# Performance work log

Measured on AMD Instinct MI355X. Metric: run time of the kernel, lower is better.

## Reference

```python
import jax, jax.numpy as jnp
import numpy as np

TEMPERATURE = 0.07
EPS = 1e-12  # matches torch F.normalize eps
B, D = 16384, 128


def setup_inputs() -> dict:
    key = jax.random.key(0)
    k1, k2 = jax.random.split(key)
    anchor = jax.random.normal(k1, (B, D), dtype=jnp.float32)
    positive = jax.random.normal(k2, (B, D), dtype=jnp.float32)
    return {"anchor": anchor, "positive": positive}


def _l2_normalize(x):
    # torch F.normalize: x / max(||x||, eps)
    n = jnp.sqrt(jnp.sum(x * x, axis=-1, keepdims=True))
    return x / jnp.maximum(n, EPS)


def reference(anchor, positive):
    a = _l2_normalize(anchor)          # [B, D]
    p = _l2_normalize(positive)        # [B, D]
    pos_sim = jnp.sum(a * p, axis=-1) / TEMPERATURE            # [B]
    sim = jnp.matmul(a, p.T) / TEMPERATURE                     # [B, B]
    neg_inf = jnp.finfo(sim.dtype).min
    bsz = sim.shape[0]
    eye = jnp.eye(bsz, dtype=bool)
    neg_sim = jnp.where(eye, neg_inf, sim)                     # diag masked
    logits = jnp.concatenate([pos_sim[:, None], neg_sim], axis=1)  # [B, B+1]
    # cross-entropy with label 0: -log_softmax(logits)[:, 0]
    lse = jax.nn.logsumexp(logits, axis=1)
    loss = lse - logits[:, 0]
    return jnp.mean(loss)
```

## Files before the change

### kernel.cpp

```cpp
#include <hip/hip_runtime.h>
#include <stdint.h>

#define NROWS 16384
#define DIM 128

typedef __attribute__((ext_vector_type(8))) __bf16 bf16x8;
typedef __attribute__((ext_vector_type(4))) float f32x4;
typedef __attribute__((ext_vector_type(4))) unsigned int u32x4;

constexpr float TEMP_INV = 1.0f / 0.07f;
constexpr float LOG2E = 1.4426950408889634f;
constexpr float LN2 = 0.69314718055994531f;
constexpr float KAPPA = LOG2E * TEMP_INV;
constexpr float SQRT_KAPPA = 4.53981600f;

__device__ __forceinline__ ushort f2bf(float x) {
  uint32_t u = __builtin_bit_cast(uint32_t, x);
  uint32_t r = (u + 0x7fffu + ((u >> 16) & 1u)) >> 16;
  return (ushort)r;
}

__device__ __forceinline__ void gload_lds16(const void* g, void* l) {
  __builtin_amdgcn_global_load_lds(
      (const __attribute__((address_space(1))) unsigned int*)g,
      (__attribute__((address_space(3))) unsigned int*)l, 16, 0, 0);
}

__global__ __launch_bounds__(256) void prep_kernel(
    const float* __restrict__ anchor, const float* __restrict__ positive,
    ushort* __restrict__ abar, ushort* __restrict__ pbar,
    float* __restrict__ pos_u)
{
  const int tid = threadIdx.x;
  const int row = blockIdx.x * 16 + (tid >> 4);
  const int c0 = (tid & 15) * 8;

  const float4* a4 = reinterpret_cast<const float4*>(anchor + (size_t)row * DIM + c0);
  const float4* p4 = reinterpret_cast<const float4*>(positive + (size_t)row * DIM + c0);
  float4 a0 = a4[0], a1 = a4[1];
  float4 p0 = p4[0], p1 = p4[1];

  float af[8] = {a0.x, a0.y, a0.z, a0.w, a1.x, a1.y, a1.z, a1.w};
  float pf[8] = {p0.x, p0.y, p0.z, p0.w, p1.x, p1.y, p1.z, p1.w};

  float sa = 0.f, sp = 0.f, dp = 0.f;
#pragma unroll
  for (int j = 0; j < 8; ++j) {
    sa += af[j] * af[j];
    sp += pf[j] * pf[j];
    dp += af[j] * pf[j];
  }
#pragma unroll
  for (int m = 1; m <= 8; m <<= 1) {
    sa += __shfl_xor(sa, m, 64);
    sp += __shfl_xor(sp, m, 64);
    dp += __shfl_xor(dp, m, 64);
  }
  float inva = 1.0f / fmaxf(sqrtf(sa), 1e-12f);
  float invp = 1.0f / fmaxf(sqrtf(sp), 1e-12f);
  float ca = inva * SQRT_KAPPA;
  float cp = invp * SQRT_KAPPA;

  ushort ua[8], up[8];
#pragma unroll
  for (int j = 0; j < 8; ++j) {
    ua[j] = f2bf(af[j] * ca);
    up[j] = f2bf(pf[j] * cp);
  }
  *reinterpret_cast<uint4*>(abar + (size_t)row * DIM + c0) = *reinterpret_cast<uint4*>(ua);
  *reinterpret_cast<uint4*>(pbar + (size_t)row * DIM + c0) = *reinterpret_cast<uint4*>(up);

  if ((tid & 15) == 0)
    pos_u[row] = dp * inva * invp * KAPPA;
}

#define NSPLIT 16
#define BM 256
#define CPB (NROWS / NSPLIT)
#define BN 32
#define NIT (CPB / BN)
#define NBUF 4
#define TILE_B (BN * 256)

__global__ __launch_bounds__(256, 3) void lse_kernel(
    const ushort* __restrict__ abar,
    const ushort* __restrict__ pbar,
    float* __restrict__ sbuf )
{
  __shared__ alignas(16) char lds[NBUF][TILE_B];

  const int tid = threadIdx.x;
  const int l = tid & 63;
  const int w = tid >> 6;
  const int r15 = l & 15;
  const int hi = l >> 4;

  const int bid = blockIdx.x;
  const int csplit = bid & 15;
  const int rowblk = bid >> 4;
  const int row0 = rowblk * BM + w * 64;
  const int col0 = csplit * CPB;

  const char* abase = (const char*)abar;
  const char* pbase = (const char*)pbar;

  bf16x8 afrag[4][4];
#pragma unroll
  for (int rg = 0; rg < 4; ++rg)
#pragma unroll
    for (int kk = 0; kk < 4; ++kk) {
      size_t off = (size_t)(row0 + rg * 16 + r15) * 256 + (size_t)(kk * 32 + hi * 8) * 2;
      u32x4 v = *reinterpret_cast<const u32x4*>(abase + off);
      afrag[rg][kk] = __builtin_bit_cast(bf16x8, v);
    }

  float s[4][4];
#pragma unroll
  for (int rg = 0; rg < 4; ++rg)
#pragma unroll
    for (int rr = 0; rr < 4; ++rr) s[rg][rr] = 0.f;

  const int trow = tid >> 4;
  const size_t src0 = (size_t)(col0 + trow) * 256 + (size_t)(((tid & 15) ^ (trow & 7)) * 16);
  char* const lds0 = &lds[0][0] + w * 1024;

#define STAGE(t)                                                              \
  do {                                                                        \
    const char* gsrc = pbase + src0 + (size_t)(t) * TILE_B;                   \
    char* ld = lds0 + (size_t)((t) & 3) * TILE_B;                             \
    gload_lds16(gsrc, ld);                                                    \
    gload_lds16(gsrc + 4096, ld + 4096);                                      \
  } while (0)

  STAGE(0);
  __builtin_amdgcn_sched_barrier(0);
  STAGE(1);
  __builtin_amdgcn_sched_barrier(0);

  for (int it = 0; it < NIT; ++it) {
    if (it < NIT - 1) {
      asm volatile("s_waitcnt vmcnt(2)" ::: "memory");
    } else {
      asm volatile("s_waitcnt vmcnt(0)" ::: "memory");
    }
    __builtin_amdgcn_s_barrier();
    asm volatile("" ::: "memory");
    __builtin_amdgcn_sched_barrier(0);

    if (it + 2 < NIT) STAGE(it + 2);

    const char* bufp = &lds[0][0] + (size_t)(it & 3) * TILE_B;
#pragma unroll
    for (int ctg = 0; ctg < 2; ++ctg) {
      const int tr = ctg * 16 + r15;
      const int sw = (tr & 7) << 4;
      const char* base = bufp + tr * 256;
      bf16x8 bfrag[4];
#pragma unroll
      for (int kk = 0; kk < 4; ++kk) {
        const int cb = kk * 64 + hi * 16;
        u32x4 v = *reinterpret_cast<const u32x4*>(base + (cb ^ sw));
        bfrag[kk] = __builtin_bit_cast(bf16x8, v);
      }
      __builtin_amdgcn_s_setprio(1);
#pragma unroll
      for (int rg = 0; rg < 4; ++rg) {
        f32x4 acc = {0.f, 0.f, 0.f, 0.f};
#pragma unroll
        for (int kk = 0; kk < 4; ++kk)
          acc = __builtin_amdgcn_mfma_f32_16x16x32_bf16(afrag[rg][kk], bfrag[kk], acc, 0, 0, 0);
        s[rg][0] += __builtin_amdgcn_exp2f(acc[0]);
        s[rg][1] += __builtin_amdgcn_exp2f(acc[1]);
        s[rg][2] += __builtin_amdgcn_exp2f(acc[2]);
        s[rg][3] += __builtin_amdgcn_exp2f(acc[3]);
      }
      __builtin_amdgcn_s_setprio(0);
    }
  }
#undef STAGE

#pragma unroll
  for (int rg = 0; rg < 4; ++rg)
#pragma unroll
    for (int rr = 0; rr < 4; ++rr) {
      float v = s[rg][rr];
      v += __shfl_xor(v, 1, 64);
      v += __shfl_xor(v, 2, 64);
      v += __shfl_xor(v, 4, 64);
      v += __shfl_xor(v, 8, 64);
      if (r15 == 0) {
        int grow = row0 + rg * 16 + hi * 4 + rr;
        sbuf[(size_t)csplit * NROWS + grow] = v;
      }
    }
}

__global__ __launch_bounds__(256) void finalize1(
    const float* __restrict__ sbuf, const float* __restrict__ pos_u,
    float* __restrict__ partial)
{
  const int tid = threadIdx.x;
  const int r = blockIdx.x * 256 + tid;
  float ssum = 0.f;
#pragma unroll
  for (int c = 0; c < NSPLIT; ++c) ssum += sbuf[(size_t)c * NROWS + r];
  float acc = LN2 * (__builtin_amdgcn_logf(ssum) - pos_u[r]);
#pragma unroll
  for (int m = 1; m <= 32; m <<= 1) acc += __shfl_xor(acc, m, 64);
  __shared__ float red[4];
  if ((tid & 63) == 0) red[tid >> 6] = acc;
  __syncthreads();
  if (tid == 0) partial[blockIdx.x] = red[0] + red[1] + red[2] + red[3];
}

__global__ __launch_bounds__(64) void finalize2(
    const float* __restrict__ partial, float* __restrict__ out)
{
  float v = partial[threadIdx.x];
#pragma unroll
  for (int m = 1; m <= 32; m <<= 1) v += __shfl_xor(v, m, 64);
  if (threadIdx.x == 0) out[0] = v * (1.0f / (float)NROWS);
}

extern "C" void kernel_launch(void* const* d_in, const int* in_sizes, int n_in,
                              void* d_out, int out_size, void* d_ws, size_t ws_size,
                              hipStream_t stream) {
  const float* anchor = (const float*)d_in[0];
  const float* positive = (const float*)d_in[1];
  char* ws = (char*)d_ws;

  ushort* abar = (ushort*)ws;
  ushort* pbar = (ushort*)(ws + (size_t)NROWS * DIM * 2);
  float* pos_u = (float*)(ws + (size_t)NROWS * DIM * 4);
  float* sbuf = (float*)(ws + (size_t)NROWS * DIM * 4 + (size_t)NROWS * 4);
  float* partial = (float*)(ws + (size_t)NROWS * DIM * 4 + (size_t)NROWS * 4
                            + (size_t)NSPLIT * NROWS * 4);
  float* out = (float*)d_out;

  prep_kernel<<<NROWS / 16, 256, 0, stream>>>(anchor, positive, abar, pbar, pos_u);
  lse_kernel<<<NSPLIT * (NROWS / BM), 256, 0, stream>>>(abar, pbar, sbuf);
  finalize1<<<NROWS / 256, 256, 0, stream>>>(sbuf, pos_u, partial);
  finalize2<<<1, 64, 0, stream>>>(partial, out);
}
```

Measured before the change: 80.73 us.

## Stage P tiles in double-buffered four-tile super-iterations with fewer barriers

The LSE kernel's pipeline changes from a ring of four 8 KB tiles, with one barrier per 32-column tile, to two 32 KB halves. Each half holds four tiles and is loaded in one burst, and the kernel synchronises twice per super-iteration, so there are fewer barriers and larger asynchronous load batches. The cost is that LDS per block grows from 32 KB to 64 KB. That likely cuts the number of resident blocks per CU below the requested three, reducing latency hiding. The loads into a half are also issued only after it has been fully consumed, behind an extra barrier.

```diff
diff --git a/kernel.cpp b/kernel.cpp
--- a/kernel.cpp
+++ b/kernel.cpp
@@ -79,15 +79,17 @@
 #define CPB (NROWS / NSPLIT)
 #define BN 32
 #define NIT (CPB / BN)
-#define NBUF 4
 #define TILE_B (BN * 256)
+#define SITILES 4
+#define NSI (NIT / SITILES)
+#define HALF_B (SITILES * TILE_B)
 
 __global__ __launch_bounds__(256, 3) void lse_kernel(
     const ushort* __restrict__ abar,
     const ushort* __restrict__ pbar,
     float* __restrict__ sbuf )
 {
-  __shared__ alignas(16) char lds[NBUF][TILE_B];
+  __shared__ alignas(16) char lds[2][HALF_B];
 
   const int tid = threadIdx.x;
   const int l = tid & 63;
@@ -122,24 +124,28 @@
 
   const int trow = tid >> 4;
   const size_t src0 = (size_t)(col0 + trow) * 256 + (size_t)(((tid & 15) ^ (trow & 7)) * 16);
-  char* const lds0 = &lds[0][0] + w * 1024;
-
-#define STAGE(t)                                                              \
+  char* const ldsbase = &lds[0][0];
+  const int w1024 = w * 1024;
+
+#define STAGE_SI(si, h)                                                       \
   do {                                                                        \
-    const char* gsrc = pbase + src0 + (size_t)(t) * TILE_B;                   \
-    char* ld = lds0 + (size_t)((t) & 3) * TILE_B;                             \
-    gload_lds16(gsrc, ld);                                                    \
-    gload_lds16(gsrc + 4096, ld + 4096);                                      \
+    const char* gs = pbase + src0 + (size_t)(si) * HALF_B;                    \
+    char* ld = ldsbase + (size_t)(h) * HALF_B + w1024;                        \
+    _Pragma("unroll")                                                         \
+    for (int t = 0; t < SITILES; ++t) {                                       \
+      gload_lds16(gs + t * TILE_B, ld + t * TILE_B);                          \
+      gload_lds16(gs + t * TILE_B + 4096, ld + t * TILE_B + 4096);            \
+    }                                                                         \
   } while (0)
 
-  STAGE(0);
+  STAGE_SI(0, 0);
   __builtin_amdgcn_sched_barrier(0);
-  STAGE(1);
+  STAGE_SI(1, 1);
   __builtin_amdgcn_sched_barrier(0);
 
-  for (int it = 0; it < NIT; ++it) {
-    if (it < NIT - 1) {
-      asm volatile("s_waitcnt vmcnt(2)" ::: "memory");
+  for (int si = 0; si < NSI; ++si) {
+    if (si < NSI - 1) {
+      asm volatile("s_waitcnt vmcnt(8)" ::: "memory");
     } else {
       asm volatile("s_waitcnt vmcnt(0)" ::: "memory");
     }
@@ -147,37 +153,45 @@
     asm volatile("" ::: "memory");
     __builtin_amdgcn_sched_barrier(0);
 
-    if (it + 2 < NIT) STAGE(it + 2);
-
-    const char* bufp = &lds[0][0] + (size_t)(it & 3) * TILE_B;
-#pragma unroll
-    for (int ctg = 0; ctg < 2; ++ctg) {
-      const int tr = ctg * 16 + r15;
-      const int sw = (tr & 7) << 4;
-      const char* base = bufp + tr * 256;
-      bf16x8 bfrag[4];
-#pragma unroll
-      for (int kk = 0; kk < 4; ++kk) {
-        const int cb = kk * 64 + hi * 16;
-        u32x4 v = *reinterpret_cast<const u32x4*>(base + (cb ^ sw));
-        bfrag[kk] = __builtin_bit_cast(bf16x8, v);
+    const char* hbase = ldsbase + (size_t)(si & 1) * HALF_B;
+#pragma unroll
+    for (int tt = 0; tt < SITILES; ++tt) {
+      const char* bufp = hbase + (size_t)tt * TILE_B;
+#pragma unroll
+      for (int ctg = 0; ctg < 2; ++ctg) {
+        const int tr = ctg * 16 + r15;
+        const int sw = (tr & 7) << 4;
+        const char* base = bufp + tr * 256;
+        bf16x8 bfrag[4];
+#pragma unroll
+        for (int kk = 0; kk < 4; ++kk) {
+          const int cb = kk * 64 + hi * 16;
+          u32x4 v = *reinterpret_cast<const u32x4*>(base + (cb ^ sw));
+          bfrag[kk] = __builtin_bit_cast(bf16x8, v);
+        }
+        __builtin_amdgcn_s_setprio(1);
+#pragma unroll
+        for (int rg = 0; rg < 4; ++rg) {
+          f32x4 acc = {0.f, 0.f, 0.f, 0.f};
+#pragma unroll
+          for (int kk = 0; kk < 4; ++kk)
+            acc = __builtin_amdgcn_mfma_f32_16x16x32_bf16(afrag[rg][kk], bfrag[kk], acc, 0, 0, 0);
+          s[rg][0] += __builtin_amdgcn_exp2f(acc[0]);
+          s[rg][1] += __builtin_amdgcn_exp2f(acc[1]);
+          s[rg][2] += __builtin_amdgcn_exp2f(acc[2]);
+          s[rg][3] += __builtin_amdgcn_exp2f(acc[3]);
+        }
+        __builtin_amdgcn_s_setprio(0);
       }
-      __builtin_amdgcn_s_setprio(1);
-#pragma unroll
-      for (int rg = 0; rg < 4; ++rg) {
-        f32x4 acc = {0.f, 0.f, 0.f, 0.f};
-#pragma unroll
-        for (int kk = 0; kk < 4; ++kk)
-          acc = __builtin_amdgcn_mfma_f32_16x16x32_bf16(afrag[rg][kk], bfrag[kk], acc, 0, 0, 0);
-        s[rg][0] += __builtin_amdgcn_exp2f(acc[0]);
-        s[rg][1] += __builtin_amdgcn_exp2f(acc[1]);
-        s[rg][2] += __builtin_amdgcn_exp2f(acc[2]);
-        s[rg][3] += __builtin_amdgcn_exp2f(acc[3]);
-      }
-      __builtin_amdgcn_s_setprio(0);
-    }
-  }
-#undef STAGE
+    }
+
+    __builtin_amdgcn_s_barrier();
+    asm volatile("" ::: "memory");
+    __builtin_amdgcn_sched_barrier(0);
+
+    if (si + 2 < NSI) STAGE_SI(si + 2, si & 1);
+  }
+#undef STAGE_SI
 
 #pragma unroll
   for (int rg = 0; rg < 4; ++rg)
```

New measurement: 107.2 us. +32.7%, slower.
